# Performance work log

Measured on AMD Instinct MI355X. Metric: run time of the kernel, lower is better.

The kernel has to match this reference:

```python
import jax, jax.numpy as jnp
import numpy as np

DIM = 1024
N_HEADS = 16
HEAD_DIM = DIM // N_HEADS


def setup_inputs() -> dict:
    key = jax.random.key(0)
    k_x, k_qkv_w, k_qkv_b, k_p_w, k_p_b = jax.random.split(key, 5)
    s = 1.0 / np.sqrt(DIM)
    return {
        "x": jax.random.normal(k_x, (2, 2048, DIM), dtype=jnp.float32),
        # stored as [in, out] so forward is x @ W + b (equivalent to torch Linear)
        "qkv_w": jax.random.uniform(k_qkv_w, (DIM, 3 * DIM), minval=-s, maxval=s, dtype=jnp.float32),
        "qkv_b": jax.random.uniform(k_qkv_b, (3 * DIM,), minval=-s, maxval=s, dtype=jnp.float32),
        "proj_w": jax.random.uniform(k_p_w, (DIM, DIM), minval=-s, maxval=s, dtype=jnp.float32),
        "proj_b": jax.random.uniform(k_p_b, (DIM,), minval=-s, maxval=s, dtype=jnp.float32),
    }


def reference(x, qkv_w, qkv_b, proj_w, proj_b):
    b, s, _ = x.shape
    qkv = x @ qkv_w + qkv_b                       # [b, s, 3*dim]
    q, k, v = jnp.split(qkv, 3, axis=-1)
    def split_heads(t):
        return t.reshape(b, s, N_HEADS, HEAD_DIM).transpose(0, 2, 1, 3)  # [b, h, s, d]
    q, k, v = map(split_heads, (q, k, v))
    scale = 1.0 / np.sqrt(HEAD_DIM)
    scores = jnp.einsum("bhqd,bhkd->bhqk", q, k) * scale
    attn = jax.nn.softmax(scores, axis=-1)
    out = jnp.einsum("bhqk,bhkd->bhqd", attn, v)
    out = out.transpose(0, 2, 1, 3).reshape(b, s, DIM)
    return out @ proj_w + proj_b
```

## Files before the change

kernel.cpp:

```cpp
#include <hip/hip_runtime.h>
#include <hip/hip_bf16.h>

typedef __attribute__((ext_vector_type(8))) short bf16x8;
typedef __attribute__((ext_vector_type(4))) float f32x4;
typedef __attribute__((ext_vector_type(16))) float f32x16;
typedef __attribute__((ext_vector_type(4))) unsigned short u16x4;
typedef __attribute__((ext_vector_type(8))) unsigned short u16x8v;

#define S_LEN 2048
#define NHEAD 16
#define HDIM 64
#define DIM 1024

__device__ __forceinline__ unsigned short f2bf(float f) {
    union { float f; unsigned u; } x; x.f = f;
    unsigned r = x.u + 0x7FFFu + ((x.u >> 16) & 1u);
    return (unsigned short)(r >> 16);
}
__device__ __forceinline__ unsigned short f2bf_fast(float f) {
    union { float f; unsigned u; } x; x.f = f;
    return (unsigned short)((x.u + 0x8000u) >> 16);
}

__device__ __forceinline__ f32x4 mfma16(bf16x8 a, bf16x8 b, f32x4 c) {
    return __builtin_amdgcn_mfma_f32_16x16x32_bf16(a, b, c, 0, 0, 0);
}
__device__ __forceinline__ f32x16 mfma32(bf16x8 a, bf16x8 b, f32x16 c) {
    return __builtin_amdgcn_mfma_f32_32x32x16_bf16(a, b, c, 0, 0, 0);
}

__device__ __forceinline__ float fexp2(float x) {
#if __has_builtin(__builtin_amdgcn_exp2f)
    return __builtin_amdgcn_exp2f(x);
#else
    return exp2f(x);
#endif
}

__device__ __forceinline__ void gl_lds16(const void* g, void* l) {
    __builtin_amdgcn_global_load_lds(
        (const __attribute__((address_space(1))) unsigned int*)g,
        (__attribute__((address_space(3))) unsigned int*)l, 16, 0, 0);
}

__global__ __launch_bounds__(256) void xconv_kernel(const float* __restrict__ X,
                                                    unsigned short* __restrict__ Xb) {
    size_t i = ((size_t)blockIdx.x * 256 + threadIdx.x) * 8;
    float4 a = *reinterpret_cast<const float4*>(&X[i]);
    float4 b = *reinterpret_cast<const float4*>(&X[i + 4]);
    u16x8v o;
    o[0] = f2bf(a.x); o[1] = f2bf(a.y); o[2] = f2bf(a.z); o[3] = f2bf(a.w);
    o[4] = f2bf(b.x); o[5] = f2bf(b.y); o[6] = f2bf(b.z); o[7] = f2bf(b.w);
    *reinterpret_cast<u16x8v*>(&Xb[i]) = o;
}

__global__ __launch_bounds__(256) void wtrans_kernel(const float* __restrict__ W,
                                                     unsigned short* __restrict__ Wt,
                                                     int K, int N) {
    __shared__ float lds[64][65];
    int k0 = blockIdx.x * 64, n0 = blockIdx.y * 64;
    int tid = threadIdx.x;
    for (int idx = tid; idx < 1024; idx += 256) {
        int row = idx >> 4, c = (idx & 15) << 2;
        float4 v = *reinterpret_cast<const float4*>(&W[(size_t)(k0 + row) * N + n0 + c]);
        lds[row][c] = v.x; lds[row][c + 1] = v.y; lds[row][c + 2] = v.z; lds[row][c + 3] = v.w;
    }
    __syncthreads();
    for (int idx = tid; idx < 1024; idx += 256) {
        int row = idx >> 4, c = (idx & 15) << 2;
        u16x4 o;
        o[0] = f2bf(lds[c][row]);     o[1] = f2bf(lds[c + 1][row]);
        o[2] = f2bf(lds[c + 2][row]); o[3] = f2bf(lds[c + 3][row]);
        *reinterpret_cast<u16x4*>(&Wt[(size_t)(n0 + row) * K + k0 + c]) = o;
    }
}

template <int MODE>
__global__ __launch_bounds__(256) void gemm_kernel(
    const unsigned short* __restrict__ Ab, const unsigned short* __restrict__ Bt,
    const float* __restrict__ bias,
    unsigned short* __restrict__ Qb, unsigned short* __restrict__ Kb,
    unsigned short* __restrict__ Vt, float* __restrict__ outf) {
    __shared__ unsigned short Alds[128 * 64];
    __shared__ unsigned short Blds[128 * 64];
    const int tid = threadIdx.x;
    const int m0 = blockIdx.x * 128, n0 = blockIdx.y * 128;
    const int wid = tid >> 6, lane = tid & 63;
    const int wm = wid >> 1, wn = wid & 1;
    const int lr = lane & 15, lg = lane >> 4;

    const char* Abase = (const char*)(Ab + (size_t)m0 * 1024);
    const char* Bbase = (const char*)(Bt + (size_t)n0 * 1024);

    int srcOff[4], dstOff[4];
#pragma unroll
    for (int i = 0; i < 4; ++i) {
        int off = i * 4096 + wid * 1024 + lane * 16;
        int row = off >> 7, col = off & 127;
        srcOff[i] = row * 2048 + (col ^ ((row & 7) << 4));
        dstOff[i] = off;
    }
    const int swz = (lr & 7) << 4;

    f32x4 acc[4][4] = {};

    for (int kt = 0; kt < 16; ++kt) {
        __syncthreads();
#pragma unroll
        for (int i = 0; i < 4; ++i) {
            gl_lds16(Abase + srcOff[i] + kt * 128, (char*)Alds + dstOff[i]);
            gl_lds16(Bbase + srcOff[i] + kt * 128, (char*)Blds + dstOff[i]);
        }
        __syncthreads();

#pragma unroll
        for (int ks = 0; ks < 2; ++ks) {
            bf16x8 af[4], bfr[4];
#pragma unroll
            for (int i = 0; i < 4; ++i)
                af[i] = *reinterpret_cast<const bf16x8*>(
                    (const char*)Alds + (wm * 64 + i * 16 + lr) * 128 + ((ks * 64 + lg * 16) ^ swz));
#pragma unroll
            for (int j = 0; j < 4; ++j)
                bfr[j] = *reinterpret_cast<const bf16x8*>(
                    (const char*)Blds + (wn * 64 + j * 16 + lr) * 128 + ((ks * 64 + lg * 16) ^ swz));
            __builtin_amdgcn_s_setprio(1);
#pragma unroll
            for (int i = 0; i < 4; ++i)
#pragma unroll
                for (int j = 0; j < 4; ++j)
                    acc[i][j] = mfma16(af[i], bfr[j], acc[i][j]);
            __builtin_amdgcn_s_setprio(0);
        }
    }

    if constexpr (MODE == 0) {
        const int sec = n0 >> 10;
#pragma unroll
        for (int j = 0; j < 4; ++j) {
            int gn = n0 + wn * 64 + j * 16 + lr;
            float bv = bias[gn];
            int nn = gn & 1023, h = nn >> 6, d = nn & 63;
#pragma unroll
            for (int i = 0; i < 4; ++i) {
#pragma unroll
                for (int r = 0; r < 4; ++r) {
                    int m = m0 + wm * 64 + i * 16 + lg * 4 + r;
                    int b_ = m >> 11, s_ = m & 2047;
                    size_t bh = (size_t)(b_ * NHEAD + h);
                    float v = acc[i][j][r] + bv;
                    if (sec == 0)
                        Qb[(bh * S_LEN + s_) * HDIM + d] = f2bf(v * 0.18033688f);
                    else if (sec == 1)
                        Kb[(bh * S_LEN + s_) * HDIM + d] = f2bf(v);
                    else
                        Vt[(bh * HDIM + d) * S_LEN + s_] = f2bf(v);
                }
            }
        }
    } else {
#pragma unroll
        for (int j = 0; j < 4; ++j) {
            int gn = n0 + wn * 64 + j * 16 + lr;
            float bv = bias[gn];
#pragma unroll
            for (int i = 0; i < 4; ++i) {
#pragma unroll
                for (int r = 0; r < 4; ++r) {
                    int m = m0 + wm * 64 + i * 16 + lg * 4 + r;
                    outf[(size_t)m * DIM + gn] = acc[i][j][r] + bv;
                }
            }
        }
    }
}

__device__ __forceinline__ void repack32(const f32x16& p, bf16x8 (&pa)[2]) {
#pragma unroll
    for (int k2 = 0; k2 < 2; ++k2) {
        const int rb = 8 * k2;
        unsigned aw[2], bw[2];
#pragma unroll
        for (int u = 0; u < 2; ++u) {
            unsigned a, b;
            asm("v_cvt_pk_bf16_f32 %0, %1, %2"
                : "=v"(a) : "v"(p[rb + 2 * u]), "v"(p[rb + 2 * u + 1]));
            asm("v_cvt_pk_bf16_f32 %0, %1, %2"
                : "=v"(b) : "v"(p[rb + 4 + 2 * u]), "v"(p[rb + 4 + 2 * u + 1]));
            asm volatile("v_permlane32_swap_b32 %0, %1" : "+v"(a), "+v"(b));
            aw[u] = a; bw[u] = b;
        }
        union { unsigned w[4]; bf16x8 v; } pu;
        pu.w[0] = aw[0]; pu.w[1] = aw[1]; pu.w[2] = bw[0]; pu.w[3] = bw[1];
        pa[k2] = pu.v;
    }
}

#define NPAIR 16
__global__ __launch_bounds__(256) void attn_kernel(const unsigned short* __restrict__ Qb,
                                                   const unsigned short* __restrict__ Kb,
                                                   const unsigned short* __restrict__ Vt,
                                                   unsigned short* __restrict__ Ob) {
    __shared__ char smem[65536];
    const int L = blockIdx.x;
    const int xcd = L & 7, slot = L >> 3;
    const int bh = xcd + 8 * (slot & 3);
    const int qblk = slot >> 2;
    const int wid = threadIdx.x >> 6;
    const int lane = threadIdx.x & 63;
    const int l31 = lane & 31, hi = lane >> 5;
    const int qh = wid & 1, kh = wid >> 1;
    const int q0 = qblk * 128 + qh * 64;

    bf16x8 qf[2][4];
#pragma unroll
    for (int s = 0; s < 2; ++s) {
        const unsigned short* qrow = &Qb[((size_t)bh * S_LEN + q0 + s * 32 + l31) * HDIM];
#pragma unroll
        for (int kst = 0; kst < 4; ++kst)
            qf[s][kst] = *reinterpret_cast<const bf16x8*>(&qrow[kst * 16 + hi * 8]);
    }

    const char* kT = (const char*)&Kb[(size_t)bh * S_LEN * HDIM];
    const char* vT = (const char*)&Vt[(size_t)bh * HDIM * S_LEN];

    const char* sbase = (wid < 2) ? kT : vT;
    const int pairStride = (wid < 2) ? 16384 : 256;
    int srcOff[8], dstOff[8];
#pragma unroll
    for (int i = 0; i < 8; ++i) {
        int id = 8 * wid + i;
        if (id < 16) {
            int t2 = (id >> 3) & 1, khs = (id >> 2) & 1, kst = id & 3;
            srcOff[i] = t2 * 8192 + (khs * 32 + l31) * 128 + kst * 32 + hi * 16;
        } else {
            int c = id - 16;
            int t2 = (c >> 3) & 1, khs = (c >> 2) & 1, dt = (c >> 1) & 1, k2 = c & 1;
            srcOff[i] = t2 * 128 + (dt * 32 + l31) * 4096 + khs * 64 + k2 * 32 + hi * 16;
        }
        dstOff[i] = id * 1024;
    }

    float ls0 = 0.f, ls1 = 0.f;
    f32x16 acc[2][2] = {};

#pragma unroll
    for (int i = 0; i < 8; ++i)
        gl_lds16(sbase + srcOff[i], smem + dstOff[i]);
    __syncthreads();

    int cur = 0;
    for (int pt = 0; pt < NPAIR; ++pt) {
        if (pt + 1 < NPAIR) {
#pragma unroll
            for (int i = 0; i < 8; ++i)
                gl_lds16(sbase + (pt + 1) * pairStride + srcOff[i],
                         smem + (cur ^ 1) * 32768 + dstOff[i]);
        }
#pragma unroll
        for (int t2 = 0; t2 < 2; ++t2) {
            const char* kbb = smem + cur * 32768 + (t2 * 8 + kh * 4) * 1024 + lane * 16;
            const char* vbb = smem + cur * 32768 + 16384 + (t2 * 8 + kh * 4) * 1024 + lane * 16;
            bf16x8 kb[4];
#pragma unroll
            for (int kst = 0; kst < 4; ++kst)
                kb[kst] = *reinterpret_cast<const bf16x8*>(kbb + kst * 1024);

            f32x16 p0 = {}, p1 = {};
            __builtin_amdgcn_s_setprio(1);
#pragma unroll
            for (int kst = 0; kst < 4; ++kst) p0 = mfma32(kb[kst], qf[0][kst], p0);
#pragma unroll
            for (int kst = 0; kst < 4; ++kst) p1 = mfma32(kb[kst], qf[1][kst], p1);
            __builtin_amdgcn_s_setprio(0);

#pragma unroll
            for (int r = 0; r < 16; ++r) {
                float e0 = fexp2(p0[r]); p0[r] = e0; ls0 += e0;
                float e1 = fexp2(p1[r]); p1[r] = e1; ls1 += e1;
            }
            bf16x8 paA[2], paB[2];
            repack32(p0, paA);
            repack32(p1, paB);

            __builtin_amdgcn_s_setprio(1);
#pragma unroll
            for (int dt = 0; dt < 2; ++dt)
#pragma unroll
                for (int k2 = 0; k2 < 2; ++k2) {
                    bf16x8 vb = *reinterpret_cast<const bf16x8*>(vbb + (dt * 2 + k2) * 1024);
                    acc[0][dt] = mfma32(paA[k2], vb, acc[0][dt]);
                    acc[1][dt] = mfma32(paB[k2], vb, acc[1][dt]);
                }
            __builtin_amdgcn_s_setprio(0);
        }
        __syncthreads();
        cur ^= 1;
    }

    ls0 += __shfl_xor(ls0, 32, 64);
    ls1 += __shfl_xor(ls1, 32, 64);

    float* cacc = (float*)smem;
    float* cls  = (float*)(smem + 32768);
    if (kh == 1) {
#pragma unroll
        for (int s = 0; s < 2; ++s)
#pragma unroll
            for (int dt = 0; dt < 2; ++dt)
#pragma unroll
                for (int r = 0; r < 16; ++r)
                    cacc[qh * 4096 + (s * 2 + dt) * 1024 + r * 64 + lane] = acc[s][dt][r];
        cls[qh * 128 + l31] = ls0;
        cls[qh * 128 + 64 + l31] = ls1;
    }
    __syncthreads();
    if (kh == 0) {
        ls0 += cls[qh * 128 + l31];
        ls1 += cls[qh * 128 + 64 + l31];
#pragma unroll
        for (int s = 0; s < 2; ++s)
#pragma unroll
            for (int dt = 0; dt < 2; ++dt)
#pragma unroll
                for (int r = 0; r < 16; ++r)
                    acc[s][dt][r] += cacc[qh * 4096 + (s * 2 + dt) * 1024 + r * 64 + lane];

        const int b_ = bh >> 4, h = bh & 15;
        float inv0[16], inv1[16];
#pragma unroll
        for (int r = 0; r < 16; ++r) {
            int rq = (r & 3) + 8 * (r >> 2) + 4 * hi;
            inv0[r] = 1.f / __shfl(ls0, rq, 64);
            inv1[r] = 1.f / __shfl(ls1, rq, 64);
        }
#pragma unroll
        for (int dt = 0; dt < 2; ++dt)
#pragma unroll
            for (int r = 0; r < 16; ++r) {
                int rq = (r & 3) + 8 * (r >> 2) + 4 * hi;
                int q0s = q0 + rq;
                Ob[((size_t)(b_ * S_LEN + q0s)) * DIM + h * HDIM + dt * 32 + l31] =
                    f2bf_fast(acc[0][dt][r] * inv0[r]);
                Ob[((size_t)(b_ * S_LEN + q0s + 32)) * DIM + h * HDIM + dt * 32 + l31] =
                    f2bf_fast(acc[1][dt][r] * inv1[r]);
            }
    }
}

extern "C" void kernel_launch(void* const* d_in, const int* in_sizes, int n_in,
                              void* d_out, int out_size, void* d_ws, size_t ws_size,
                              hipStream_t stream) {
    const float* x      = (const float*)d_in[0];
    const float* qkv_w  = (const float*)d_in[1];
    const float* qkv_b  = (const float*)d_in[2];
    const float* proj_w = (const float*)d_in[3];
    const float* proj_b = (const float*)d_in[4];
    float* out = (float*)d_out;

    unsigned short* Wqkvt = (unsigned short*)d_ws;
    unsigned short* Wpt   = Wqkvt + 3072 * 1024;
    unsigned short* Qb    = Wpt + 1024 * 1024;
    unsigned short* Kb    = Qb + 32 * 2048 * 64;
    unsigned short* Vt    = Kb + 32 * 2048 * 64;
    unsigned short* Ob    = Vt + 32 * 2048 * 64;
    unsigned short* Xb    = Ob + 4096 * 1024;

    xconv_kernel<<<2048, 256, 0, stream>>>(x, Xb);
    wtrans_kernel<<<dim3(16, 48), 256, 0, stream>>>(qkv_w, Wqkvt, 1024, 3072);
    wtrans_kernel<<<dim3(16, 16), 256, 0, stream>>>(proj_w, Wpt, 1024, 1024);

    gemm_kernel<0><<<dim3(32, 24), 256, 0, stream>>>(Xb, Wqkvt, qkv_b, Qb, Kb, Vt, nullptr);
    attn_kernel<<<512, 256, 0, stream>>>(Qb, Kb, Vt, Ob);
    gemm_kernel<1><<<dim3(32, 8), 256, 0, stream>>>(Ob, Wpt, proj_b, nullptr, nullptr, nullptr, out);
}
```

Before: 120.9 us.

## Split attention block across 8 waves with 32 query rows each

The attention kernel now launches 512 threads per block, and each wave handles 32 query rows instead of 64. Each wave does half the MFMA work and holds half the accumulators and Q fragments. Loading of K/V tiles into LDS is spread over 8 waves with 4 loads each instead of 8. The aim is more waves per CU to hide latency and cut register pressure. In exchange, every K fragment is now read from LDS by twice as many waves, so per-FLOP LDS read traffic doubles, and block-wide barriers cover more waves.

```diff
diff --git a/kernel.cpp b/kernel.cpp
--- a/kernel.cpp
+++ b/kernel.cpp
@@ -197,10 +197,10 @@
 }
 
 #define NPAIR 16
-__global__ __launch_bounds__(256) void attn_kernel(const unsigned short* __restrict__ Qb,
-                                                   const unsigned short* __restrict__ Kb,
-                                                   const unsigned short* __restrict__ Vt,
-                                                   unsigned short* __restrict__ Ob) {
+__global__ __launch_bounds__(512, 4) void attn_kernel(const unsigned short* __restrict__ Qb,
+                                                      const unsigned short* __restrict__ Kb,
+                                                      const unsigned short* __restrict__ Vt,
+                                                      unsigned short* __restrict__ Ob) {
     __shared__ char smem[65536];
     const int L = blockIdx.x;
     const int xcd = L & 7, slot = L >> 3;
@@ -209,27 +209,24 @@
     const int wid = threadIdx.x >> 6;
     const int lane = threadIdx.x & 63;
     const int l31 = lane & 31, hi = lane >> 5;
-    const int qh = wid & 1, kh = wid >> 1;
-    const int q0 = qblk * 128 + qh * 64;
-
-    bf16x8 qf[2][4];
-#pragma unroll
-    for (int s = 0; s < 2; ++s) {
-        const unsigned short* qrow = &Qb[((size_t)bh * S_LEN + q0 + s * 32 + l31) * HDIM];
-#pragma unroll
-        for (int kst = 0; kst < 4; ++kst)
-            qf[s][kst] = *reinterpret_cast<const bf16x8*>(&qrow[kst * 16 + hi * 8]);
-    }
+    const int qs = wid & 3, kh = wid >> 2;
+    const int q0 = qblk * 128 + qs * 32;
+
+    const unsigned short* qrow = &Qb[((size_t)bh * S_LEN + q0 + l31) * HDIM];
+    bf16x8 qf[4];
+#pragma unroll
+    for (int kst = 0; kst < 4; ++kst)
+        qf[kst] = *reinterpret_cast<const bf16x8*>(&qrow[kst * 16 + hi * 8]);
 
     const char* kT = (const char*)&Kb[(size_t)bh * S_LEN * HDIM];
     const char* vT = (const char*)&Vt[(size_t)bh * HDIM * S_LEN];
 
-    const char* sbase = (wid < 2) ? kT : vT;
-    const int pairStride = (wid < 2) ? 16384 : 256;
-    int srcOff[8], dstOff[8];
-#pragma unroll
-    for (int i = 0; i < 8; ++i) {
-        int id = 8 * wid + i;
+    const char* sbase = (wid < 4) ? kT : vT;
+    const int pairStride = (wid < 4) ? 16384 : 256;
+    int srcOff[4], dstOff[4];
+#pragma unroll
+    for (int i = 0; i < 4; ++i) {
+        int id = 4 * wid + i;
         if (id < 16) {
             int t2 = (id >> 3) & 1, khs = (id >> 2) & 1, kst = id & 3;
             srcOff[i] = t2 * 8192 + (khs * 32 + l31) * 128 + kst * 32 + hi * 16;
@@ -241,11 +238,11 @@
         dstOff[i] = id * 1024;
     }
 
-    float ls0 = 0.f, ls1 = 0.f;
-    f32x16 acc[2][2] = {};
-
-#pragma unroll
-    for (int i = 0; i < 8; ++i)
+    float ls = 0.f;
+    f32x16 acc[2] = {};
+
+#pragma unroll
+    for (int i = 0; i < 4; ++i)
         gl_lds16(sbase + srcOff[i], smem + dstOff[i]);
     __syncthreads();
 
@@ -253,7 +250,7 @@
     for (int pt = 0; pt < NPAIR; ++pt) {
         if (pt + 1 < NPAIR) {
 #pragma unroll
-            for (int i = 0; i < 8; ++i)
+            for (int i = 0; i < 4; ++i)
                 gl_lds16(sbase + (pt + 1) * pairStride + srcOff[i],
                          smem + (cur ^ 1) * 32768 + dstOff[i]);
         }
@@ -261,27 +258,22 @@
         for (int t2 = 0; t2 < 2; ++t2) {
             const char* kbb = smem + cur * 32768 + (t2 * 8 + kh * 4) * 1024 + lane * 16;
             const char* vbb = smem + cur * 32768 + 16384 + (t2 * 8 + kh * 4) * 1024 + lane * 16;
-            bf16x8 kb[4];
-#pragma unroll
-            for (int kst = 0; kst < 4; ++kst)
-                kb[kst] = *reinterpret_cast<const bf16x8*>(kbb + kst * 1024);
-
-            f32x16 p0 = {}, p1 = {};
+
+            f32x16 p = {};
             __builtin_amdgcn_s_setprio(1);
 #pragma unroll
-            for (int kst = 0; kst < 4; ++kst) p0 = mfma32(kb[kst], qf[0][kst], p0);
-#pragma unroll
-            for (int kst = 0; kst < 4; ++kst) p1 = mfma32(kb[kst], qf[1][kst], p1);
+            for (int kst = 0; kst < 4; ++kst) {
+                bf16x8 kb = *reinterpret_cast<const bf16x8*>(kbb + kst * 1024);
+                p = mfma32(kb, qf[kst], p);
+            }
             __builtin_amdgcn_s_setprio(0);
 
 #pragma unroll
             for (int r = 0; r < 16; ++r) {
-                float e0 = fexp2(p0[r]); p0[r] = e0; ls0 += e0;
-                float e1 = fexp2(p1[r]); p1[r] = e1; ls1 += e1;
-            }
-            bf16x8 paA[2], paB[2];
-            repack32(p0, paA);
-            repack32(p1, paB);
+                float e = fexp2(p[r]); p[r] = e; ls += e;
+            }
+            bf16x8 pa[2];
+            repack32(p, pa);
 
             __builtin_amdgcn_s_setprio(1);
 #pragma unroll
@@ -289,8 +281,7 @@
 #pragma unroll
                 for (int k2 = 0; k2 < 2; ++k2) {
                     bf16x8 vb = *reinterpret_cast<const bf16x8*>(vbb + (dt * 2 + k2) * 1024);
-                    acc[0][dt] = mfma32(paA[k2], vb, acc[0][dt]);
-                    acc[1][dt] = mfma32(paB[k2], vb, acc[1][dt]);
+                    acc[dt] = mfma32(pa[k2], vb, acc[dt]);
                 }
             __builtin_amdgcn_s_setprio(0);
         }
@@ -298,52 +289,42 @@
         cur ^= 1;
     }
 
-    ls0 += __shfl_xor(ls0, 32, 64);
-    ls1 += __shfl_xor(ls1, 32, 64);
+    ls += __shfl_xor(ls, 32, 64);
 
     float* cacc = (float*)smem;
     float* cls  = (float*)(smem + 32768);
     if (kh == 1) {
 #pragma unroll
-        for (int s = 0; s < 2; ++s)
-#pragma unroll
-            for (int dt = 0; dt < 2; ++dt)
-#pragma unroll
-                for (int r = 0; r < 16; ++r)
-                    cacc[qh * 4096 + (s * 2 + dt) * 1024 + r * 64 + lane] = acc[s][dt][r];
-        cls[qh * 128 + l31] = ls0;
-        cls[qh * 128 + 64 + l31] = ls1;
+        for (int dt = 0; dt < 2; ++dt)
+#pragma unroll
+            for (int r = 0; r < 16; ++r)
+                cacc[qs * 2048 + dt * 1024 + r * 64 + lane] = acc[dt][r];
+        cls[qs * 32 + l31] = ls;
     }
     __syncthreads();
     if (kh == 0) {
-        ls0 += cls[qh * 128 + l31];
-        ls1 += cls[qh * 128 + 64 + l31];
-#pragma unroll
-        for (int s = 0; s < 2; ++s)
-#pragma unroll
-            for (int dt = 0; dt < 2; ++dt)
-#pragma unroll
-                for (int r = 0; r < 16; ++r)
-                    acc[s][dt][r] += cacc[qh * 4096 + (s * 2 + dt) * 1024 + r * 64 + lane];
+        ls += cls[qs * 32 + l31];
+#pragma unroll
+        for (int dt = 0; dt < 2; ++dt)
+#pragma unroll
+            for (int r = 0; r < 16; ++r)
+                acc[dt][r] += cacc[qs * 2048 + dt * 1024 + r * 64 + lane];
 
         const int b_ = bh >> 4, h = bh & 15;
-        float inv0[16], inv1[16];
+        float inv[16];
 #pragma unroll
         for (int r = 0; r < 16; ++r) {
             int rq = (r & 3) + 8 * (r >> 2) + 4 * hi;
-            inv0[r] = 1.f / __shfl(ls0, rq, 64);
-            inv1[r] = 1.f / __shfl(ls1, rq, 64);
+            inv[r] = 1.f / __shfl(ls, rq, 64);
         }
 #pragma unroll
         for (int dt = 0; dt < 2; ++dt)
 #pragma unroll
             for (int r = 0; r < 16; ++r) {
                 int rq = (r & 3) + 8 * (r >> 2) + 4 * hi;
-                int q0s = q0 + rq;
-                Ob[((size_t)(b_ * S_LEN + q0s)) * DIM + h * HDIM + dt * 32 + l31] =
-                    f2bf_fast(acc[0][dt][r] * inv0[r]);
-                Ob[((size_t)(b_ * S_LEN + q0s + 32)) * DIM + h * HDIM + dt * 32 + l31] =
-                    f2bf_fast(acc[1][dt][r] * inv1[r]);
+                int q = q0 + rq;
+                Ob[((size_t)(b_ * S_LEN + q)) * DIM + h * HDIM + dt * 32 + l31] =
+                    f2bf_fast(acc[dt][r] * inv[r]);
             }
     }
 }
@@ -371,6 +352,6 @@
     wtrans_kernel<<<dim3(16, 16), 256, 0, stream>>>(proj_w, Wpt, 1024, 1024);
 
     gemm_kernel<0><<<dim3(32, 24), 256, 0, stream>>>(Xb, Wqkvt, qkv_b, Qb, Kb, Vt, nullptr);
-    attn_kernel<<<512, 256, 0, stream>>>(Qb, Kb, Vt, Ob);
+    attn_kernel<<<512, 512, 0, stream>>>(Qb, Kb, Vt, Ob);
     gemm_kernel<1><<<dim3(32, 8), 256, 0, stream>>>(Ob, Wpt, proj_b, nullptr, nullptr, nullptr, out);
 }
```

New measurement: 114.5 us. -5.3%, faster.
